# Kernel optimization log

Hardware: AMD Instinct MI355X
Metric: run time of the kernel (lower is better)

Reference implementation:

```python
import jax, jax.numpy as jnp
import numpy as np

B, K, T, C = 4, 8, 2048, 64

def setup_inputs() -> dict:
    key = jax.random.key(0)
    ks = jax.random.split(key, 7)
    return {
        "x": jax.random.normal(ks[0], (B, K, T, C), dtype=jnp.float32),
        "Wq": jax.random.normal(ks[1], (C, C), dtype=jnp.float32) / np.sqrt(C),
        "bq": jax.random.normal(ks[2], (C,), dtype=jnp.float32) * 0.01,
        "Wk": jax.random.normal(ks[3], (C, C), dtype=jnp.float32) / np.sqrt(C),
        "bk": jax.random.normal(ks[4], (C,), dtype=jnp.float32) * 0.01,
        "Wv": jax.random.normal(ks[5], (C, C), dtype=jnp.float32) / np.sqrt(C),
        "bv": jax.random.normal(ks[6], (C,), dtype=jnp.float32) * 0.01,
    }

def reference(x, Wq, bq, Wk, bk, Wv, bv):
    c_dim = x.shape[-1]
    # torch nn.Linear: y = x @ W.T + b
    q = jnp.einsum('bktc,dc->bktd', x, Wq) + bq
    k = jnp.einsum('bktc,dc->bktd', x, Wk) + bk
    v = jnp.einsum('bktc,dc->bktd', x, Wv) + bv
    scores = jnp.einsum('bkic,bkjc->bkij', q, k) / jnp.sqrt(jnp.float32(c_dim))
    attn = jax.nn.softmax(scores, axis=-1)
    out = jnp.einsum('bkij,bkjc->bkic', attn, v)
    return out
```

## Files before the change

kernel.cpp:

```cpp
#include <hip/hip_runtime.h>


#define T_DIM 2048
#define NHEAD 32
#define HSTRIDE (T_DIM * 64)
#define QSCALE 0.18033688011112042f
#define SOFF  8.0f

#define SWZ(row, grp) ((row) * 64 + ((((grp) ^ ((row) & 7)) & 7) * 8))

typedef _Float16 h8 __attribute__((ext_vector_type(8)));
typedef _Float16 h4 __attribute__((ext_vector_type(4)));
typedef __fp16   g2 __attribute__((ext_vector_type(2)));
typedef float    f4 __attribute__((ext_vector_type(4)));

union H4U { h4 v; g2 p[2]; };
union H8U { h8 v; h4 h[2]; };

#if defined(__has_builtin)
#if __has_builtin(__builtin_amdgcn_exp2f)
#define EXP2(x) __builtin_amdgcn_exp2f(x)
#endif
#endif
#ifndef EXP2
__device__ inline float exp2_raw(float x) {
    float r;
    asm("v_exp_f32 %0, %1" : "=v"(r) : "v"(x));
    return r;
}
#define EXP2(x) exp2_raw(x)
#endif

__device__ inline h4 cvt4(f4 x) {
    H4U u;
    u.p[0] = __builtin_amdgcn_cvt_pkrtz(x[0], x[1]);
    u.p[1] = __builtin_amdgcn_cvt_pkrtz(x[2], x[3]);
    return u.v;
}

__device__ inline h8 cvt8(f4 a, f4 b) {
    H8U r;
    r.h[0] = cvt4(a);
    r.h[1] = cvt4(b);
    return r.v;
}

__global__ __launch_bounds__(256) void qkv_proj_kernel(
    const float* __restrict__ x,
    const float* __restrict__ Wq, const float* __restrict__ bq,
    const float* __restrict__ Wk, const float* __restrict__ bk,
    const float* __restrict__ Wv, const float* __restrict__ bv,
    _Float16* __restrict__ qh, _Float16* __restrict__ khT,
    _Float16* __restrict__ vtT)
{
    __shared__ _Float16 ws[3][64 * 64];
    __shared__ _Float16 ot[64 * 64];
    __shared__ float bsh[3][64];

    const int tid  = threadIdx.x;
    const int row0 = blockIdx.x * 64;
    const int head = blockIdx.x >> 5;
    const int t0   = (blockIdx.x & 31) * 64;

    #pragma unroll
    for (int m = 0; m < 3; ++m) {
        const float* Wm = (m == 0) ? Wq : ((m == 1) ? Wk : Wv);
        const float* bm = (m == 0) ? bq : ((m == 1) ? bk : bv);
        #pragma unroll
        for (int pass = 0; pass < 4; ++pass) {
            const int idx = pass * 1024 + tid * 4;
            const int d = idx >> 6, c = idx & 63;
            f4 wv = *(const f4*)(Wm + idx);
            *(h4*)&ws[m][SWZ(d, c >> 3) + (c & 7)] = cvt4(wv);
        }
        if (tid < 64) bsh[m][tid] = bm[tid];
    }

    const int w    = tid >> 6;
    const int lane = tid & 63;
    const int l15  = lane & 15;
    const int qd   = lane >> 4;

    h8 af[2];
    {
        const float* xp = x + (size_t)(row0 + w * 16 + l15) * 64 + qd * 8;
        #pragma unroll
        for (int ch = 0; ch < 2; ++ch) {
            f4 a0 = *(const f4*)(xp + ch * 32);
            f4 a1 = *(const f4*)(xp + ch * 32 + 4);
            af[ch] = cvt8(a0, a1);
        }
    }
    __syncthreads();

    #pragma unroll
    for (int m = 0; m < 3; ++m) {
        h8 bf[4][2];
        #pragma unroll
        for (int ns = 0; ns < 4; ++ns)
            #pragma unroll
            for (int ch = 0; ch < 2; ++ch)
                bf[ns][ch] = *(const h8*)&ws[m][SWZ(ns * 16 + l15, ch * 4 + qd)];

        f4 acc[4];
        #pragma unroll
        for (int ns = 0; ns < 4; ++ns)
            acc[ns] = (f4){0.f, 0.f, 0.f, 0.f};
        #pragma unroll
        for (int ch = 0; ch < 2; ++ch)
            #pragma unroll
            for (int ns = 0; ns < 4; ++ns)
                acc[ns] = __builtin_amdgcn_mfma_f32_16x16x32_f16(
                    af[ch], bf[ns][ch], acc[ns], 0, 0, 0);

        __syncthreads();
        if (m < 2) {
            #pragma unroll
            for (int ns = 0; ns < 4; ++ns) {
                const int d = ns * 16 + l15;
                const float bias = bsh[m][d];
                #pragma unroll
                for (int r = 0; r < 4; ++r) {
                    const int t = w * 16 + qd * 4 + r;
                    float v = acc[ns][r] + bias;
                    if (m == 0) v *= QSCALE;
                    ot[SWZ(t, d >> 3) + (d & 7)] = (_Float16)v;
                }
            }
            __syncthreads();
            if (m == 0) {
                #pragma unroll
                for (int pass = 0; pass < 2; ++pass) {
                    const int t  = pass * 32 + (tid >> 3);
                    const int c0 = (tid & 7) * 8;
                    *(h8*)&qh[(size_t)(row0 + t) * 64 + c0] =
                        *(const h8*)&ot[SWZ(t, tid & 7)];
                }
            } else {
                #pragma unroll
                for (int pass = 0; pass < 2; ++pass) {
                    const int f    = pass * 2048 + tid * 8;
                    const int Jl   = f >> 10;
                    const int rest = f & 1023;
                    const int ch_  = rest >> 9;
                    const int qd_  = (rest >> 7) & 3;
                    const int l15_ = (rest >> 3) & 15;
                    h8 val = *(const h8*)&ot[SWZ(Jl * 16 + l15_, ch_ * 4 + qd_)];
                    *(h8*)&khT[(size_t)head * HSTRIDE + ((t0 >> 4) + Jl) * 1024 + rest] = val;
                }
            }
        } else {
            #pragma unroll
            for (int ns = 0; ns < 4; ++ns) {
                const int d = ns * 16 + l15;
                const float bias = bsh[2][d];
                const int tl = w * 16 + qd * 4;
                f4 pvf;
                #pragma unroll
                for (int r = 0; r < 4; ++r)
                    pvf[r] = acc[ns][r] + bias;
                *(h4*)&ot[SWZ(d, tl >> 3) + (tl & 7)] = cvt4(pvf);
            }
            __syncthreads();
            #pragma unroll
            for (int pass = 0; pass < 2; ++pass) {
                const int f   = pass * 2048 + tid * 8;
                const int qd3 = f >> 10;
                const int rem = f & 1023;
                const int c   = rem >> 4;
                const int g   = (rem & 15) >> 3;
                const int ta  = (2 * g) * 16 + qd3 * 4;
                const int tb  = ta + 16;
                H8U val;
                val.h[0] = *(const h4*)&ot[SWZ(c, ta >> 3) + (ta & 7)];
                val.h[1] = *(const h4*)&ot[SWZ(c, tb >> 3) + (tb & 7)];
                *(h8*)&vtT[(size_t)head * HSTRIDE + (t0 >> 6) * 4096 + f] = val.v;
            }
        }
    }
}

__global__ __launch_bounds__(256, 2) void attn_kernel(
    const _Float16* __restrict__ qh, const _Float16* __restrict__ khT,
    const _Float16* __restrict__ vtT, float* __restrict__ out)
{
    __shared__ float mrg[2][64][35];
    const int tid  = threadIdx.x;
    const int w    = tid >> 6;
    const int lane = tid & 63;
    const int l15  = lane & 15;
    const int qd   = lane >> 4;
    const int qgrp = w >> 1;
    const int kph  = w & 1;

    const int bid  = blockIdx.x;
    const int xcd  = bid & 7;
    const int slot = bid >> 3;
    const int head = xcd * 4 + (slot >> 5);
    const int q0   = (slot & 31) * 64 + qgrp * 32;

    h8 qf[2][2];
    #pragma unroll
    for (int is = 0; is < 2; ++is) {
        const _Float16* qp = qh + (size_t)(head * T_DIM + q0 + is * 16 + l15) * 64 + qd * 8;
        qf[is][0] = *(const h8*)qp;
        qf[is][1] = *(const h8*)(qp + 32);
    }

    f4 rs4[2] = {(f4){0.f,0.f,0.f,0.f}, (f4){0.f,0.f,0.f,0.f}};
    f4 oacc[2][4];
    #pragma unroll
    for (int is = 0; is < 2; ++is)
        #pragma unroll
        for (int cs = 0; cs < 4; ++cs)
            oacc[is][cs] = (f4){0.f, 0.f, 0.f, 0.f};

    const _Float16* kA = khT + (size_t)head * HSTRIDE + kph * 65536;
    const _Float16* kB = kA + 2048;
    const _Float16* vA = vtT + (size_t)head * HSTRIDE + kph * 65536;
    const int ko = lane * 8;
    const int vo = qd * 1024 + l15 * 16;

    h8 kf[4][2];
    #pragma unroll
    for (int jt = 0; jt < 4; ++jt)
        #pragma unroll
        for (int ch = 0; ch < 2; ++ch)
            kf[jt][ch] = *(const h8*)(((jt < 2) ? kA : kB) + (jt & 1) * 1024 + ch * 512 + ko);

    for (int kt = 0; kt < 16; ++kt) {
        H8U vf8[4][2];
        #pragma unroll
        for (int cs = 0; cs < 4; ++cs) {
            vf8[cs][0].v = *(const h8*)(vA + cs * 256 + vo);
            vf8[cs][1].v = *(const h8*)(vA + cs * 256 + vo + 8);
        }

        f4 st[4][2];
        #pragma unroll
        for (int jt = 0; jt < 4; ++jt)
            #pragma unroll
            for (int is = 0; is < 2; ++is)
                st[jt][is] = (f4){-SOFF, -SOFF, -SOFF, -SOFF};
        #pragma unroll
        for (int ch = 0; ch < 2; ++ch)
            #pragma unroll
            for (int jt = 0; jt < 4; ++jt)
                #pragma unroll
                for (int is = 0; is < 2; ++is)
                    st[jt][is] = __builtin_amdgcn_mfma_f32_16x16x32_f16(
                        kf[jt][ch], qf[is][ch], st[jt][is], 0, 0, 0);

        kA += 4096; kB += 4096;
        if (kt < 15) {
            #pragma unroll
            for (int jt = 0; jt < 4; ++jt)
                #pragma unroll
                for (int ch = 0; ch < 2; ++ch)
                    kf[jt][ch] = *(const h8*)(((jt < 2) ? kA : kB) + (jt & 1) * 1024 + ch * 512 + ko);
        }

        h4 pf[4][2];
        #pragma unroll
        for (int is = 0; is < 2; ++is)
            #pragma unroll
            for (int jt = 0; jt < 4; ++jt) {
                f4 p;
                p[0] = EXP2(st[jt][is][0]);
                p[1] = EXP2(st[jt][is][1]);
                p[2] = EXP2(st[jt][is][2]);
                p[3] = EXP2(st[jt][is][3]);
                rs4[is] += p;
                pf[jt][is] = cvt4(p);
            }

        #pragma unroll
        for (int jt = 0; jt < 4; ++jt)
            #pragma unroll
            for (int cs = 0; cs < 4; ++cs)
                #pragma unroll
                for (int is = 0; is < 2; ++is)
                    oacc[is][cs] = __builtin_amdgcn_mfma_f32_16x16x16f16(
                        pf[jt][is], vf8[cs][jt >> 1].h[jt & 1], oacc[is][cs], 0, 0, 0);

        vA += 4096;
    }

    float lx[2];
    #pragma unroll
    for (int is = 0; is < 2; ++is) {
        float l = (rs4[is][0] + rs4[is][1]) + (rs4[is][2] + rs4[is][3]);
        l += __shfl_xor(l, 16, 64);
        l += __shfl_xor(l, 32, 64);
        lx[is] = l;
    }

    if (kph == 1) {
        #pragma unroll
        for (int is = 0; is < 2; ++is) {
            #pragma unroll
            for (int cs = 0; cs < 4; ++cs)
                #pragma unroll
                for (int r = 0; r < 4; ++r)
                    mrg[qgrp][lane][(is * 4 + cs) * 4 + r] = oacc[is][cs][r];
            mrg[qgrp][lane][32 + is] = lx[is];
        }
    }
    __syncthreads();
    if (kph == 0) {
        #pragma unroll
        for (int is = 0; is < 2; ++is) {
            const float linvv = 1.f / (lx[is] + mrg[qgrp][lane][32 + is]);
            float linv[4];
            #pragma unroll
            for (int r = 0; r < 4; ++r)
                linv[r] = __shfl(linvv, qd * 4 + r, 64);
            #pragma unroll
            for (int cs = 0; cs < 4; ++cs) {
                const int c = cs * 16 + l15;
                #pragma unroll
                for (int r = 0; r < 4; ++r) {
                    const int t = q0 + is * 16 + qd * 4 + r;
                    float o = oacc[is][cs][r] + mrg[qgrp][lane][(is * 4 + cs) * 4 + r];
                    out[(size_t)(head * T_DIM + t) * 64 + c] = o * linv[r];
                }
            }
        }
    }
}

extern "C" void kernel_launch(void* const* d_in, const int* in_sizes, int n_in,
                              void* d_out, int out_size, void* d_ws, size_t ws_size,
                              hipStream_t stream)
{
    (void)in_sizes; (void)n_in; (void)out_size; (void)ws_size;
    const float* x  = (const float*)d_in[0];
    const float* Wq = (const float*)d_in[1];
    const float* bq = (const float*)d_in[2];
    const float* Wk = (const float*)d_in[3];
    const float* bk = (const float*)d_in[4];
    const float* Wv = (const float*)d_in[5];
    const float* bv = (const float*)d_in[6];
    float* out = (float*)d_out;

    _Float16* qh  = (_Float16*)d_ws;
    _Float16* khT = qh + (size_t)NHEAD * HSTRIDE;
    _Float16* vtT = khT + (size_t)NHEAD * HSTRIDE;

    hipLaunchKernelGGL(qkv_proj_kernel, dim3(1024), dim3(256), 0, stream,
                       x, Wq, bq, Wk, bk, Wv, bv, qh, khT, vtT);
    hipLaunchKernelGGL(attn_kernel, dim3(1024), dim3(256), 0, stream,
                       qh, khT, vtT, out);
}
```

Baseline: 129.8 us.

## Warp-specialize attention with producer waves staging K/V tiles through shared memory

The attention kernel is restructured into 6 waves per block. Two producer waves load K and V tiles from global memory into a double-buffered shared-memory ring, and four consumer waves each process 32 queries over all keys, which removes the split-K merge step. The grid is halved to 512 blocks of 128 queries, so K/V fetched once per block is reused by four consumer waves instead of each wave reading it directly from global. The cost is a block-wide barrier every tile, barrier counts that must match between producers and consumers, and lower occupancy since the launch bound drops the 2-blocks hint.

```diff
diff --git a/kernel.cpp b/kernel.cpp
--- a/kernel.cpp
+++ b/kernel.cpp
@@ -8,6 +8,8 @@
 #define SOFF  8.0f
 
 #define SWZ(row, grp) ((row) * 64 + ((((grp) ^ ((row) & 7)) & 7) * 8))
+
+#define RAW_BARRIER() asm volatile("s_waitcnt lgkmcnt(0)\n\ts_barrier" ::: "memory")
 
 typedef _Float16 h8 __attribute__((ext_vector_type(8)));
 typedef _Float16 h4 __attribute__((ext_vector_type(4)));
@@ -180,137 +182,109 @@
     }
 }
 
-__global__ __launch_bounds__(256, 2) void attn_kernel(
+__global__ __launch_bounds__(384) void attn_kernel(
     const _Float16* __restrict__ qh, const _Float16* __restrict__ khT,
     const _Float16* __restrict__ vtT, float* __restrict__ out)
 {
-    __shared__ float mrg[2][64][35];
+    __shared__ _Float16 tiles[2][8192];
     const int tid  = threadIdx.x;
     const int w    = tid >> 6;
     const int lane = tid & 63;
     const int l15  = lane & 15;
     const int qd   = lane >> 4;
-    const int qgrp = w >> 1;
-    const int kph  = w & 1;
 
     const int bid  = blockIdx.x;
     const int xcd  = bid & 7;
     const int slot = bid >> 3;
-    const int head = xcd * 4 + (slot >> 5);
-    const int q0   = (slot & 31) * 64 + qgrp * 32;
-
-    h8 qf[2][2];
-    #pragma unroll
-    for (int is = 0; is < 2; ++is) {
-        const _Float16* qp = qh + (size_t)(head * T_DIM + q0 + is * 16 + l15) * 64 + qd * 8;
-        qf[is][0] = *(const h8*)qp;
-        qf[is][1] = *(const h8*)(qp + 32);
-    }
-
-    f4 rs4[2] = {(f4){0.f,0.f,0.f,0.f}, (f4){0.f,0.f,0.f,0.f}};
-    f4 oacc[2][4];
-    #pragma unroll
-    for (int is = 0; is < 2; ++is)
-        #pragma unroll
-        for (int cs = 0; cs < 4; ++cs)
-            oacc[is][cs] = (f4){0.f, 0.f, 0.f, 0.f};
-
-    const _Float16* kA = khT + (size_t)head * HSTRIDE + kph * 65536;
-    const _Float16* kB = kA + 2048;
-    const _Float16* vA = vtT + (size_t)head * HSTRIDE + kph * 65536;
-    const int ko = lane * 8;
-    const int vo = qd * 1024 + l15 * 16;
-
-    h8 kf[4][2];
-    #pragma unroll
-    for (int jt = 0; jt < 4; ++jt)
-        #pragma unroll
-        for (int ch = 0; ch < 2; ++ch)
-            kf[jt][ch] = *(const h8*)(((jt < 2) ? kA : kB) + (jt & 1) * 1024 + ch * 512 + ko);
-
-    for (int kt = 0; kt < 16; ++kt) {
-        H8U vf8[4][2];
-        #pragma unroll
-        for (int cs = 0; cs < 4; ++cs) {
-            vf8[cs][0].v = *(const h8*)(vA + cs * 256 + vo);
-            vf8[cs][1].v = *(const h8*)(vA + cs * 256 + vo + 8);
-        }
-
-        f4 st[4][2];
-        #pragma unroll
-        for (int jt = 0; jt < 4; ++jt)
+    const int head = xcd * 4 + (slot >> 4);
+    const int qpart = slot & 15;
+
+    if (w < 4) {
+        const int q0 = qpart * 128 + w * 32;
+
+        h8 qf[2][2];
+        #pragma unroll
+        for (int is = 0; is < 2; ++is) {
+            const _Float16* qp = qh + (size_t)(head * T_DIM + q0 + is * 16 + l15) * 64 + qd * 8;
+            qf[is][0] = *(const h8*)qp;
+            qf[is][1] = *(const h8*)(qp + 32);
+        }
+
+        f4 rs4[2] = {(f4){0.f,0.f,0.f,0.f}, (f4){0.f,0.f,0.f,0.f}};
+        f4 oacc[2][4];
+        #pragma unroll
+        for (int is = 0; is < 2; ++is)
+            #pragma unroll
+            for (int cs = 0; cs < 4; ++cs)
+                oacc[is][cs] = (f4){0.f, 0.f, 0.f, 0.f};
+
+        const int ko = lane * 8;
+        __syncthreads();
+
+        for (int it = 0; it < 32; ++it) {
+            const _Float16* kb = &tiles[it & 1][0];
+            const _Float16* vb = kb + 4096;
+
+            h8 kf[4][2];
+            #pragma unroll
+            for (int jt = 0; jt < 4; ++jt)
+                #pragma unroll
+                for (int ch = 0; ch < 2; ++ch)
+                    kf[jt][ch] = *(const h8*)(kb + jt * 1024 + ch * 512 + ko);
+            H8U vf8[4][2];
+            #pragma unroll
+            for (int cs = 0; cs < 4; ++cs) {
+                vf8[cs][0].v = *(const h8*)(vb + (cs * 2 + 0) * 512 + ko);
+                vf8[cs][1].v = *(const h8*)(vb + (cs * 2 + 1) * 512 + ko);
+            }
+
+            f4 st[4][2];
+            #pragma unroll
+            for (int jt = 0; jt < 4; ++jt)
+                #pragma unroll
+                for (int is = 0; is < 2; ++is)
+                    st[jt][is] = (f4){-SOFF, -SOFF, -SOFF, -SOFF};
+            #pragma unroll
+            for (int ch = 0; ch < 2; ++ch)
+                #pragma unroll
+                for (int jt = 0; jt < 4; ++jt)
+                    #pragma unroll
+                    for (int is = 0; is < 2; ++is)
+                        st[jt][is] = __builtin_amdgcn_mfma_f32_16x16x32_f16(
+                            kf[jt][ch], qf[is][ch], st[jt][is], 0, 0, 0);
+
+            h4 pf[4][2];
             #pragma unroll
             for (int is = 0; is < 2; ++is)
-                st[jt][is] = (f4){-SOFF, -SOFF, -SOFF, -SOFF};
-        #pragma unroll
-        for (int ch = 0; ch < 2; ++ch)
+                #pragma unroll
+                for (int jt = 0; jt < 4; ++jt) {
+                    f4 p;
+                    p[0] = EXP2(st[jt][is][0]);
+                    p[1] = EXP2(st[jt][is][1]);
+                    p[2] = EXP2(st[jt][is][2]);
+                    p[3] = EXP2(st[jt][is][3]);
+                    rs4[is] += p;
+                    pf[jt][is] = cvt4(p);
+                }
+
             #pragma unroll
             for (int jt = 0; jt < 4; ++jt)
                 #pragma unroll
-                for (int is = 0; is < 2; ++is)
-                    st[jt][is] = __builtin_amdgcn_mfma_f32_16x16x32_f16(
-                        kf[jt][ch], qf[is][ch], st[jt][is], 0, 0, 0);
-
-        kA += 4096; kB += 4096;
-        if (kt < 15) {
-            #pragma unroll
-            for (int jt = 0; jt < 4; ++jt)
-                #pragma unroll
-                for (int ch = 0; ch < 2; ++ch)
-                    kf[jt][ch] = *(const h8*)(((jt < 2) ? kA : kB) + (jt & 1) * 1024 + ch * 512 + ko);
-        }
-
-        h4 pf[4][2];
-        #pragma unroll
-        for (int is = 0; is < 2; ++is)
-            #pragma unroll
-            for (int jt = 0; jt < 4; ++jt) {
-                f4 p;
-                p[0] = EXP2(st[jt][is][0]);
-                p[1] = EXP2(st[jt][is][1]);
-                p[2] = EXP2(st[jt][is][2]);
-                p[3] = EXP2(st[jt][is][3]);
-                rs4[is] += p;
-                pf[jt][is] = cvt4(p);
-            }
-
-        #pragma unroll
-        for (int jt = 0; jt < 4; ++jt)
-            #pragma unroll
-            for (int cs = 0; cs < 4; ++cs)
-                #pragma unroll
-                for (int is = 0; is < 2; ++is)
-                    oacc[is][cs] = __builtin_amdgcn_mfma_f32_16x16x16f16(
-                        pf[jt][is], vf8[cs][jt >> 1].h[jt & 1], oacc[is][cs], 0, 0, 0);
-
-        vA += 4096;
-    }
-
-    float lx[2];
-    #pragma unroll
-    for (int is = 0; is < 2; ++is) {
-        float l = (rs4[is][0] + rs4[is][1]) + (rs4[is][2] + rs4[is][3]);
-        l += __shfl_xor(l, 16, 64);
-        l += __shfl_xor(l, 32, 64);
-        lx[is] = l;
-    }
-
-    if (kph == 1) {
+                for (int cs = 0; cs < 4; ++cs)
+                    #pragma unroll
+                    for (int is = 0; is < 2; ++is)
+                        oacc[is][cs] = __builtin_amdgcn_mfma_f32_16x16x16f16(
+                            pf[jt][is], vf8[cs][jt >> 1].h[jt & 1], oacc[is][cs], 0, 0, 0);
+
+            __syncthreads();
+        }
+
         #pragma unroll
         for (int is = 0; is < 2; ++is) {
-            #pragma unroll
-            for (int cs = 0; cs < 4; ++cs)
-                #pragma unroll
-                for (int r = 0; r < 4; ++r)
-                    mrg[qgrp][lane][(is * 4 + cs) * 4 + r] = oacc[is][cs][r];
-            mrg[qgrp][lane][32 + is] = lx[is];
-        }
-    }
-    __syncthreads();
-    if (kph == 0) {
-        #pragma unroll
-        for (int is = 0; is < 2; ++is) {
-            const float linvv = 1.f / (lx[is] + mrg[qgrp][lane][32 + is]);
+            float l = (rs4[is][0] + rs4[is][1]) + (rs4[is][2] + rs4[is][3]);
+            l += __shfl_xor(l, 16, 64);
+            l += __shfl_xor(l, 32, 64);
+            const float linvv = 1.f / l;
             float linv[4];
             #pragma unroll
             for (int r = 0; r < 4; ++r)
@@ -321,10 +295,76 @@
                 #pragma unroll
                 for (int r = 0; r < 4; ++r) {
                     const int t = q0 + is * 16 + qd * 4 + r;
-                    float o = oacc[is][cs][r] + mrg[qgrp][lane][(is * 4 + cs) * 4 + r];
-                    out[(size_t)(head * T_DIM + t) * 64 + c] = o * linv[r];
-                }
-            }
+                    out[(size_t)(head * T_DIM + t) * 64 + c] = oacc[is][cs][r] * linv[r];
+                }
+            }
+        }
+    } else if (w == 4) {
+        const _Float16* kT = khT + (size_t)head * HSTRIDE;
+        const int lo = lane * 8;
+        h8 sA[8], sB[8];
+        #pragma unroll
+        for (int b = 0; b < 8; ++b) sA[b] = *(const h8*)(kT + b * 512 + lo);
+        #pragma unroll
+        for (int b = 0; b < 8; ++b) sB[b] = *(const h8*)(kT + 4096 + b * 512 + lo);
+        const _Float16* kp = kT + 8192;
+        #pragma unroll
+        for (int b = 0; b < 8; ++b) *(h8*)(&tiles[0][0] + b * 512 + lo) = sA[b];
+        RAW_BARRIER();
+
+        for (int it2 = 0; it2 < 16; ++it2) {
+            if (it2 < 15) {
+                #pragma unroll
+                for (int b = 0; b < 8; ++b) sA[b] = *(const h8*)(kp + b * 512 + lo);
+                kp += 4096;
+            }
+            #pragma unroll
+            for (int b = 0; b < 8; ++b) *(h8*)(&tiles[1][0] + b * 512 + lo) = sB[b];
+            RAW_BARRIER();
+            if (it2 < 15) {
+                #pragma unroll
+                for (int b = 0; b < 8; ++b) sB[b] = *(const h8*)(kp + b * 512 + lo);
+                kp += 4096;
+                #pragma unroll
+                for (int b = 0; b < 8; ++b) *(h8*)(&tiles[0][0] + b * 512 + lo) = sA[b];
+            }
+            RAW_BARRIER();
+        }
+    } else {
+        const _Float16* vT = vtT + (size_t)head * HSTRIDE;
+        const int lo  = lane * 8;
+        const int voA = (lane >> 4) * 1024 + (lane & 15) * 16;
+        h8 sA[8], sB[8];
+        #pragma unroll
+        for (int b = 0; b < 8; ++b)
+            sA[b] = *(const h8*)(vT + voA + (b >> 1) * 256 + (b & 1) * 8);
+        #pragma unroll
+        for (int b = 0; b < 8; ++b)
+            sB[b] = *(const h8*)(vT + 4096 + voA + (b >> 1) * 256 + (b & 1) * 8);
+        const _Float16* vp = vT + 8192;
+        #pragma unroll
+        for (int b = 0; b < 8; ++b) *(h8*)(&tiles[0][4096] + b * 512 + lo) = sA[b];
+        RAW_BARRIER();
+
+        for (int it2 = 0; it2 < 16; ++it2) {
+            if (it2 < 15) {
+                #pragma unroll
+                for (int b = 0; b < 8; ++b)
+                    sA[b] = *(const h8*)(vp + voA + (b >> 1) * 256 + (b & 1) * 8);
+                vp += 4096;
+            }
+            #pragma unroll
+            for (int b = 0; b < 8; ++b) *(h8*)(&tiles[1][4096] + b * 512 + lo) = sB[b];
+            RAW_BARRIER();
+            if (it2 < 15) {
+                #pragma unroll
+                for (int b = 0; b < 8; ++b)
+                    sB[b] = *(const h8*)(vp + voA + (b >> 1) * 256 + (b & 1) * 8);
+                vp += 4096;
+                #pragma unroll
+                for (int b = 0; b < 8; ++b) *(h8*)(&tiles[0][4096] + b * 512 + lo) = sA[b];
+            }
+            RAW_BARRIER();
         }
     }
 }
@@ -349,6 +389,6 @@
 
     hipLaunchKernelGGL(qkv_proj_kernel, dim3(1024), dim3(256), 0, stream,
                        x, Wq, bq, Wk, bk, Wv, bv, qh, khT, vtT);
-    hipLaunchKernelGGL(attn_kernel, dim3(1024), dim3(256), 0, stream,
+    hipLaunchKernelGGL(attn_kernel, dim3(512), dim3(384), 0, stream,
                        qh, khT, vtT, out);
 }
```

After: 128.0 us. About the same (-1.4%).
